# Performance work log

Measured on AMD Instinct MI355X. Metric: run time of the kernel, lower is better.

The kernel has to match this reference:

```python
import jax, jax.numpy as jnp
import numpy as np

HEADS = 8
UNITS = 1024
D_ATT = UNITS // HEADS  # 128
NEG_INF = -1e9  # matches Keras Attention additive causal mask


def setup_inputs() -> dict:
    key = jax.random.key(0)
    kx, kq, kk, kv, ko = jax.random.split(key, 5)
    B, T = 4, 2048
    scale = 0.02
    x = jax.random.normal(kx, (B, T, UNITS), dtype=jnp.float32)
    Wq = jax.random.normal(kq, (UNITS, HEADS * D_ATT), dtype=jnp.float32) * scale
    Wk = jax.random.normal(kk, (UNITS, HEADS * D_ATT), dtype=jnp.float32) * scale
    Wv = jax.random.normal(kv, (UNITS, D_ATT), dtype=jnp.float32) * scale
    Wo = jax.random.normal(ko, (D_ATT, UNITS), dtype=jnp.float32) * scale
    return {"x": x, "Wq": Wq, "Wk": Wk, "Wv": Wv, "Wo": Wo}


def reference(x, Wq, Wk, Wv, Wo):
    # TFT interpretable multi-head self-attention (inference; dropout inactive).
    B, T, U = x.shape
    H, d = HEADS, D_ATT
    scale = 1.0 / jnp.sqrt(jnp.asarray(d, x.dtype))  # query / sqrt(shape(key)[-1])
    q = (x @ Wq).reshape(B, T, H, d) * scale          # [B,T,H,d]
    k = (x @ Wk).reshape(B, T, H, d)                  # [B,T,H,d]
    v = x @ Wv                                        # [B,T,d], shared across heads
    scores = jnp.einsum("bthd,bshd->bhts", q, k)      # [B,H,T,T]
    causal = jnp.tril(jnp.ones((T, T), dtype=bool))   # [T,T]
    scores = jnp.where(causal, scores, jnp.asarray(NEG_INF, scores.dtype))
    w = jax.nn.softmax(scores, axis=-1)               # [B,H,T,T]
    out = jnp.einsum("bhts,bsd->bthd", w, v)          # [B,T,H,d]
    out = out.mean(axis=2) @ Wo                       # mean over heads -> Dense(units)
    attn = w.mean(axis=1)                             # mean attention over heads [B,T,T]
    return out, attn
```

## Files before the change

kernel.cpp:

```cpp
#include <hip/hip_runtime.h>

#define BATCH 4
#define TSEQ  2048
#define UNITS 1024
#define HEADS 8
#define DH    128
#define MROWS (BATCH*TSEQ)
#define NCAT  (2*UNITS + DH)

typedef short bf16x8 __attribute__((ext_vector_type(8)));
typedef short short4v __attribute__((ext_vector_type(4)));
typedef float f32x4  __attribute__((ext_vector_type(4)));

__device__ __forceinline__ short f2bf(float f){
    union { float f; unsigned u; } v; v.f = f;
    unsigned r = v.u + 0x7fff + ((v.u >> 16) & 1);
    return (short)(r >> 16);
}
__device__ __forceinline__ float redsum16(float v){
    #pragma unroll
    for (int m = 1; m < 16; m <<= 1) v += __shfl_xor(v, m);
    return v;
}
__device__ __forceinline__ void gload_lds16(const void* g, void* l){
    __builtin_amdgcn_global_load_lds(
        (const __attribute__((address_space(1))) void*)g,
        (__attribute__((address_space(3))) void*)l, 16, 0, 0);
}

#define QSCALE (0.08838834764831845f * 1.4426950408889634f)

__global__ __launch_bounds__(256) void xcast_kernel(const float* __restrict__ x,
                                                    short* __restrict__ Xbf)
{
    const int N = MROWS*UNITS/8;
    for (int i = blockIdx.x*256 + threadIdx.x; i < N; i += gridDim.x*256){
        f32x4 a = *(const f32x4*)(x + (size_t)i*8);
        f32x4 b = *(const f32x4*)(x + (size_t)i*8 + 4);
        bf16x8 o;
        o[0]=f2bf(a[0]); o[1]=f2bf(a[1]); o[2]=f2bf(a[2]); o[3]=f2bf(a[3]);
        o[4]=f2bf(b[0]); o[5]=f2bf(b[1]); o[6]=f2bf(b[2]); o[7]=f2bf(b[3]);
        *(bf16x8*)(Xbf + (size_t)i*8) = o;
    }
}

__global__ __launch_bounds__(256) void wtrans_kernel(
    const float* __restrict__ Wq, const float* __restrict__ Wk,
    const float* __restrict__ Wv, const float* __restrict__ Wo,
    short* __restrict__ WT, short* __restrict__ WoT)
{
    __shared__ float T_lds[64][65];
    const int tid = threadIdx.x;
    const int bid = blockIdx.x;
    if (bid < 544){
        const int nt = bid >> 4, kt = bid & 15;
        const int n0 = nt*64, k0 = kt*64;
        const float* src; int scol; float sc = 1.0f; int sstride = UNITS;
        if (n0 < UNITS){ src = Wq; scol = n0; sc = QSCALE; }
        else if (n0 < 2*UNITS){ src = Wk; scol = n0 - UNITS; }
        else { src = Wv; scol = n0 - 2*UNITS; sstride = DH; }
        const int ln = tid & 63, lk0 = tid >> 6;
        for (int kk = lk0; kk < 64; kk += 4)
            T_lds[kk][ln] = src[(size_t)(k0+kk)*sstride + scol + ln] * sc;
        __syncthreads();
        const int lk = tid & 63, ln0 = tid >> 6;
        for (int nn = ln0; nn < 64; nn += 4)
            WT[(size_t)(n0+nn)*UNITS + k0 + lk] = f2bf(T_lds[lk][nn]);
    } else {
        const int t = bid - 544;
        const int nt = t >> 1, dt = t & 1;
        const int n0 = nt*64, d0 = dt*64;
        const int ln = tid & 63, lk0 = tid >> 6;
        for (int dd = lk0; dd < 64; dd += 4)
            T_lds[dd][ln] = Wo[(size_t)(d0+dd)*UNITS + n0 + ln];
        __syncthreads();
        const int ld = tid & 63, ln0 = tid >> 6;
        for (int nn = ln0; nn < 64; nn += 4)
            WoT[(size_t)(n0+nn)*DH + d0 + ld] = f2bf(T_lds[ld][nn]);
    }
}

__global__ __launch_bounds__(256) void gemm_qkv_kernel(
    const short* __restrict__ X, const short* __restrict__ WT,
    short* __restrict__ Qbf, short* __restrict__ Kbf, short* __restrict__ Vt)
{
    __shared__ short A_lds[128][32];
    __shared__ short B_lds[128][32];
    const int tid = threadIdx.x;
    const int w = tid >> 6, l = tid & 63, lg = l >> 4, lr = l & 15;
    const int wm = w >> 1, wn = w & 1;
    const int n0 = blockIdx.x * 128;
    const int m0 = blockIdx.y * 128;
    const f32x4 fzero = {0.f, 0.f, 0.f, 0.f};
    f32x4 acc[4][4];
    #pragma unroll
    for (int i = 0; i < 4; i++)
        #pragma unroll
        for (int j = 0; j < 4; j++) acc[i][j] = fzero;

    const int srow = (l >> 2);
    const int scol = (l & 3) * 8;

    for (int k0 = 0; k0 < UNITS; k0 += 32){
        #pragma unroll
        for (int i = 0; i < 2; i++){
            int row = w*32 + i*16 + srow;
            gload_lds16(X  + (size_t)(m0+row)*UNITS + k0 + scol,
                        (char*)A_lds + ((w*2 + i) << 10));
            gload_lds16(WT + (size_t)(n0+row)*UNITS + k0 + scol,
                        (char*)B_lds + ((w*2 + i) << 10));
        }
        __syncthreads();
        bf16x8 af[4], bfr[4];
        #pragma unroll
        for (int mf = 0; mf < 4; mf++)
            af[mf] = *(const bf16x8*)(&A_lds[wm*64 + mf*16 + lr][lg*8]);
        #pragma unroll
        for (int nf = 0; nf < 4; nf++)
            bfr[nf] = *(const bf16x8*)(&B_lds[wn*64 + nf*16 + lr][lg*8]);
        #pragma unroll
        for (int mf = 0; mf < 4; mf++)
            #pragma unroll
            for (int nf = 0; nf < 4; nf++)
                acc[mf][nf] = __builtin_amdgcn_mfma_f32_16x16x32_bf16(
                    af[mf], bfr[nf], acc[mf][nf], 0, 0, 0);
        __syncthreads();
    }

    #pragma unroll
    for (int mf = 0; mf < 4; mf++){
        #pragma unroll
        for (int nf = 0; nf < 4; nf++){
            #pragma unroll
            for (int r = 0; r < 4; r++){
                int gr = m0 + wm*64 + mf*16 + lg*4 + r;
                int gc = n0 + wn*64 + nf*16 + lr;
                int b = gr >> 11, t = gr & 2047;
                short v = f2bf(acc[mf][nf][r]);
                if (gc < UNITS){
                    int h = gc >> 7, dd = gc & 127;
                    Qbf[(((size_t)(b*HEADS + h))*TSEQ + t)*DH + dd] = v;
                } else if (gc < 2*UNITS){
                    int h = (gc - UNITS) >> 7, dd = gc & 127;
                    Kbf[(((size_t)(b*HEADS + h))*TSEQ + t)*DH + dd] = v;
                } else {
                    int dd = gc - 2*UNITS;
                    Vt[((size_t)b*DH + dd)*TSEQ + t] = v;
                }
            }
        }
    }
}

__global__ __launch_bounds__(256) void stats_kernel(
    const short* __restrict__ Qbf, const short* __restrict__ Kbf,
    float* __restrict__ Lb)
{
    __shared__ short K_lds[2][64][136];
    const int tid = threadIdx.x;
    const int w = tid >> 6, l = tid & 63, lg = l >> 4, lr = l & 15;
    const int bh = blockIdx.y;
    const int qt = 31 - blockIdx.x;
    const int q0 = qt * 64;
    const short* Qh = Qbf + (size_t)bh*TSEQ*DH;
    const short* Kh = Kbf + (size_t)bh*TSEQ*DH;
    const f32x4 fzero = {0.f, 0.f, 0.f, 0.f};

    const int srow = tid >> 4;
    const int sc8  = tid & 15;

    const int qrow = q0 + w*16 + lr;
    bf16x8 aq[4];
    #pragma unroll
    for (int ks = 0; ks < 4; ks++)
        aq[ks] = *(const bf16x8*)(Qh + (size_t)qrow*DH + ks*32 + lg*8);

    bf16x8 kreg[4];
    #pragma unroll
    for (int i = 0; i < 4; i++)
        kreg[i] = *(const bf16x8*)(Kh + (size_t)(srow + i*16)*DH + sc8*8);
    #pragma unroll
    for (int i = 0; i < 4; i++)
        *(bf16x8*)(&K_lds[0][srow + i*16][sc8*8]) = kreg[i];
    __syncthreads();

    float lrow[4] = {0.f, 0.f, 0.f, 0.f};
    const int ntile = qt + 1;
    for (int t = 0; t < ntile; t++){
        const int cur = t & 1;
        if (t + 1 < ntile){
            const size_t base = (size_t)((t+1)*64 + srow)*DH + sc8*8;
            #pragma unroll
            for (int i = 0; i < 4; i++)
                kreg[i] = *(const bf16x8*)(Kh + base + (size_t)i*16*DH);
        }
        f32x4 sacc[4];
        #pragma unroll
        for (int nf = 0; nf < 4; nf++) sacc[nf] = fzero;
        __builtin_amdgcn_s_setprio(1);
        #pragma unroll
        for (int ks = 0; ks < 4; ks++){
            #pragma unroll
            for (int nf = 0; nf < 4; nf++){
                bf16x8 kb = *(const bf16x8*)(&K_lds[cur][nf*16 + lr][ks*32 + lg*8]);
                sacc[nf] = __builtin_amdgcn_mfma_f32_16x16x32_bf16(aq[ks], kb, sacc[nf], 0,0,0);
            }
        }
        __builtin_amdgcn_s_setprio(0);
        if (t == qt){
            #pragma unroll
            for (int nf = 0; nf < 4; nf++)
                #pragma unroll
                for (int r = 0; r < 4; r++)
                    if (nf*16 + lr > w*16 + lg*4 + r) sacc[nf][r] = -1e30f;
        }
        #pragma unroll
        for (int r = 0; r < 4; r++)
            lrow[r] += (exp2f(sacc[0][r]) + exp2f(sacc[1][r]))
                     + (exp2f(sacc[2][r]) + exp2f(sacc[3][r]));
        if (t + 1 < ntile){
            #pragma unroll
            for (int i = 0; i < 4; i++)
                *(bf16x8*)(&K_lds[cur ^ 1][srow + i*16][sc8*8]) = kreg[i];
        }
        __syncthreads();
    }
    #pragma unroll
    for (int r = 0; r < 4; r++) lrow[r] = redsum16(lrow[r]);
    if (lr == 0){
        #pragma unroll
        for (int r = 0; r < 4; r++){
            int t = q0 + w*16 + lg*4 + r;
            Lb[(size_t)bh*TSEQ + t] = 1.0f / lrow[r];
        }
    }
}

__global__ __launch_bounds__(256) void attn_kernel(
    const short* __restrict__ Qbf, const short* __restrict__ Kbf,
    const float* __restrict__ Lb, float* __restrict__ attn)
{
    const int tid = threadIdx.x;
    const int b = blockIdx.y;
    const int qt = blockIdx.x >> 5, kvt = blockIdx.x & 31;
    const int q0 = qt*128, k0 = kvt*64;
    float* At = attn + (size_t)b*TSEQ*TSEQ;

    if (k0 > q0 + 127){
        const f32x4 fz = {0.f, 0.f, 0.f, 0.f};
        #pragma unroll
        for (int i = 0; i < 8; i++){
            int c = tid + i*256;
            int row = c >> 4, c4 = c & 15;
            *(f32x4*)(At + (size_t)(q0+row)*TSEQ + k0 + c4*4) = fz;
        }
        return;
    }

    __shared__ short K_lds[2][64][136];
    const int w = tid >> 6, l = tid & 63, lg = l >> 4, lr = l & 15;
    const int srow = tid >> 4, sc8 = tid & 15;
    const f32x4 fzero = {0.f, 0.f, 0.f, 0.f};
    const size_t bh0 = (size_t)(b*HEADS)*TSEQ*DH;

    bf16x8 kreg[4];
    {
        const short* Kh = Kbf + bh0;
        #pragma unroll
        for (int i = 0; i < 4; i++)
            kreg[i] = *(const bf16x8*)(Kh + (size_t)(k0 + srow + i*16)*DH + sc8*8);
        #pragma unroll
        for (int i = 0; i < 4; i++)
            *(bf16x8*)(&K_lds[0][srow + i*16][sc8*8]) = kreg[i];
    }
    __syncthreads();

    f32x4 wacc[2][4];
    #pragma unroll
    for (int qf = 0; qf < 2; qf++)
        #pragma unroll
        for (int nf = 0; nf < 4; nf++) wacc[qf][nf] = fzero;

    for (int h = 0; h < HEADS; h++){
        const int cur = h & 1;
        if (h + 1 < HEADS){
            const short* Kn = Kbf + bh0 + (size_t)(h+1)*TSEQ*DH;
            #pragma unroll
            for (int i = 0; i < 4; i++)
                kreg[i] = *(const bf16x8*)(Kn + (size_t)(k0 + srow + i*16)*DH + sc8*8);
        }
        const short* Qh = Qbf + bh0 + (size_t)h*TSEQ*DH;
        bf16x8 aq[2][4];
        #pragma unroll
        for (int qf = 0; qf < 2; qf++)
            #pragma unroll
            for (int ks = 0; ks < 4; ks++)
                aq[qf][ks] = *(const bf16x8*)(Qh + (size_t)(q0 + w*32 + qf*16 + lr)*DH + ks*32 + lg*8);

        f32x4 sacc[2][4];
        #pragma unroll
        for (int qf = 0; qf < 2; qf++)
            #pragma unroll
            for (int nf = 0; nf < 4; nf++) sacc[qf][nf] = fzero;
        __builtin_amdgcn_s_setprio(1);
        #pragma unroll
        for (int ks = 0; ks < 4; ks++){
            #pragma unroll
            for (int nf = 0; nf < 4; nf++){
                bf16x8 kb = *(const bf16x8*)(&K_lds[cur][nf*16 + lr][ks*32 + lg*8]);
                sacc[0][nf] = __builtin_amdgcn_mfma_f32_16x16x32_bf16(aq[0][ks], kb, sacc[0][nf], 0,0,0);
                sacc[1][nf] = __builtin_amdgcn_mfma_f32_16x16x32_bf16(aq[1][ks], kb, sacc[1][nf], 0,0,0);
            }
        }
        __builtin_amdgcn_s_setprio(0);

        const float* Lh = Lb + ((size_t)(b*HEADS + h))*TSEQ;
        #pragma unroll
        for (int qf = 0; qf < 2; qf++){
            f32x4 rlh = *(const f32x4*)(Lh + q0 + w*32 + qf*16 + lg*4);
            #pragma unroll
            for (int nf = 0; nf < 4; nf++){
                #pragma unroll
                for (int r = 0; r < 4; r++){
                    int row = q0 + w*32 + qf*16 + lg*4 + r;
                    int col = k0 + nf*16 + lr;
                    float v = (col <= row) ? exp2f(sacc[qf][nf][r]) * rlh[r] : 0.f;
                    wacc[qf][nf][r] += v;
                }
            }
        }
        if (h + 1 < HEADS){
            #pragma unroll
            for (int i = 0; i < 4; i++)
                *(bf16x8*)(&K_lds[cur ^ 1][srow + i*16][sc8*8]) = kreg[i];
        }
        __syncthreads();
    }

    float* ob = (float*)&K_lds[0][0][0];
    #pragma unroll
    for (int qf = 0; qf < 2; qf++)
        #pragma unroll
        for (int nf = 0; nf < 4; nf++)
            #pragma unroll
            for (int r = 0; r < 4; r++)
                ob[(w*32 + qf*16 + lg*4 + r)*68 + nf*16 + lr] = wacc[qf][nf][r] * 0.125f;
    __syncthreads();
    #pragma unroll
    for (int i = 0; i < 8; i++){
        int c = tid + i*256;
        int row = c >> 4, c4 = c & 15;
        *(f32x4*)(At + (size_t)(q0+row)*TSEQ + k0 + c4*4) =
            *(const f32x4*)(ob + row*68 + c4*4);
    }
}

__global__ __launch_bounds__(256) void pv_kernel(
    const float* __restrict__ attn, const short* __restrict__ Vt,
    float* __restrict__ Obuf)
{
    __shared__ short A_lds[64][72];
    __shared__ short V_lds[128][72];
    const int tid = threadIdx.x;
    const int w = tid >> 6, l = tid & 63, lg = l >> 4, lr = l & 15;
    const int mt = blockIdx.x;
    const int ks0 = blockIdx.y;
    const int b = blockIdx.z;
    const int m0 = mt*64;
    const int kmax = m0 + 64;
    const int kbeg = ks0*512;
    if (kbeg >= kmax) return;
    const int kend = min(kbeg + 512, kmax);
    const int nact = (kmax + 511) >> 9;
    const float* Ab = attn + (size_t)b*TSEQ*TSEQ;
    const short* Vb = Vt + (size_t)b*DH*TSEQ;
    const f32x4 fzero = {0.f, 0.f, 0.f, 0.f};
    f32x4 acc[8];
    #pragma unroll
    for (int i = 0; i < 8; i++) acc[i] = fzero;

    for (int k0 = kbeg; k0 < kend; k0 += 64){
        #pragma unroll
        for (int i = 0; i < 4; i++){
            int c = tid + i*256;
            int row = c >> 4, c4 = c & 15;
            f32x4 av = *(const f32x4*)(Ab + (size_t)(m0+row)*TSEQ + k0 + c4*4);
            short4v o;
            o[0]=f2bf(av[0]); o[1]=f2bf(av[1]); o[2]=f2bf(av[2]); o[3]=f2bf(av[3]);
            *(short4v*)(&A_lds[row][c4*4]) = o;
        }
        #pragma unroll
        for (int i = 0; i < 4; i++){
            int c = tid + i*256;
            int row = c >> 3, c8 = c & 7;
            *(bf16x8*)(&V_lds[row][c8*8]) =
                *(const bf16x8*)(Vb + (size_t)row*TSEQ + k0 + c8*8);
        }
        __syncthreads();
        __builtin_amdgcn_s_setprio(1);
        #pragma unroll
        for (int ks = 0; ks < 2; ks++){
            bf16x8 a = *(const bf16x8*)(&A_lds[w*16 + lr][ks*32 + lg*8]);
            #pragma unroll
            for (int cg = 0; cg < 8; cg++){
                bf16x8 vb = *(const bf16x8*)(&V_lds[cg*16 + lr][ks*32 + lg*8]);
                acc[cg] = __builtin_amdgcn_mfma_f32_16x16x32_bf16(a, vb, acc[cg], 0,0,0);
            }
        }
        __builtin_amdgcn_s_setprio(0);
        __syncthreads();
    }
    #pragma unroll
    for (int cg = 0; cg < 8; cg++)
        #pragma unroll
        for (int r = 0; r < 4; r++){
            int row = m0 + w*16 + lg*4 + r, col = cg*16 + lr;
            float* p = &Obuf[((size_t)b*TSEQ + row)*DH + col];
            if (nact == 1) *p = acc[cg][r];
            else atomicAdd(p, acc[cg][r]);
        }
}

__global__ __launch_bounds__(256) void gemm_out_kernel(
    const float* __restrict__ Ob, const short* __restrict__ WoT,
    float* __restrict__ out)
{
    __shared__ short A_lds[128][40];
    __shared__ short B_lds[128][40];
    const int tid = threadIdx.x;
    const int w = tid >> 6, l = tid & 63, lg = l >> 4, lr = l & 15;
    const int wm = w >> 1, wn = w & 1;
    const int n0 = blockIdx.x * 128;
    const int m0 = blockIdx.y * 128;
    const f32x4 fzero = {0.f, 0.f, 0.f, 0.f};
    f32x4 acc[4][4];
    #pragma unroll
    for (int i = 0; i < 4; i++)
        #pragma unroll
        for (int j = 0; j < 4; j++) acc[i][j] = fzero;

    for (int k0 = 0; k0 < DH; k0 += 32){
        #pragma unroll
        for (int i = 0; i < 2; i++){
            int c = tid + i*256;
            int row = c >> 2, c8 = c & 3;
            f32x4 a0 = *(const f32x4*)(Ob + (size_t)(m0+row)*DH + k0 + c8*8);
            f32x4 a1 = *(const f32x4*)(Ob + (size_t)(m0+row)*DH + k0 + c8*8 + 4);
            bf16x8 o;
            o[0]=f2bf(a0[0]); o[1]=f2bf(a0[1]); o[2]=f2bf(a0[2]); o[3]=f2bf(a0[3]);
            o[4]=f2bf(a1[0]); o[5]=f2bf(a1[1]); o[6]=f2bf(a1[2]); o[7]=f2bf(a1[3]);
            *(bf16x8*)(&A_lds[row][c8*8]) = o;
            *(bf16x8*)(&B_lds[row][c8*8]) =
                *(const bf16x8*)(WoT + (size_t)(n0+row)*DH + k0 + c8*8);
        }
        __syncthreads();
        bf16x8 af[4], bfr[4];
        #pragma unroll
        for (int mf = 0; mf < 4; mf++)
            af[mf] = *(const bf16x8*)(&A_lds[wm*64 + mf*16 + lr][lg*8]);
        #pragma unroll
        for (int nf = 0; nf < 4; nf++)
            bfr[nf] = *(const bf16x8*)(&B_lds[wn*64 + nf*16 + lr][lg*8]);
        #pragma unroll
        for (int mf = 0; mf < 4; mf++)
            #pragma unroll
            for (int nf = 0; nf < 4; nf++)
                acc[mf][nf] = __builtin_amdgcn_mfma_f32_16x16x32_bf16(
                    af[mf], bfr[nf], acc[mf][nf], 0, 0, 0);
        __syncthreads();
    }
    #pragma unroll
    for (int mf = 0; mf < 4; mf++)
        #pragma unroll
        for (int nf = 0; nf < 4; nf++)
            #pragma unroll
            for (int r = 0; r < 4; r++){
                int gr = m0 + wm*64 + mf*16 + lg*4 + r;
                int gc = n0 + wn*64 + nf*16 + lr;
                out[(size_t)gr*UNITS + gc] = acc[mf][nf][r];
            }
}

extern "C" void kernel_launch(void* const* d_in, const int* in_sizes, int n_in,
                              void* d_out, int out_size, void* d_ws, size_t ws_size,
                              hipStream_t stream)
{
    const float* x  = (const float*)d_in[0];
    const float* Wq = (const float*)d_in[1];
    const float* Wk = (const float*)d_in[2];
    const float* Wv = (const float*)d_in[3];
    const float* Wo = (const float*)d_in[4];
    float* out  = (float*)d_out;
    float* attn = out + (size_t)MROWS*UNITS;

    char* ws = (char*)d_ws;
    short* Xbf = (short*)(ws);
    short* WT  = (short*)(ws + 16777216);
    short* Qbf = (short*)(ws + 21233664);
    short* Kbf = (short*)(ws + 38010880);
    short* Vt  = (short*)(ws + 54788096);
    float* Lb  = (float*)(ws + 57147392);
    short* WoT = (short*)(ws + 57409536);
    float* Obuf = (float*)ws;

    xcast_kernel<<<2048, 256, 0, stream>>>(x, Xbf);
    wtrans_kernel<<<576, 256, 0, stream>>>(Wq, Wk, Wv, Wo, WT, WoT);
    gemm_qkv_kernel<<<dim3(NCAT/128, MROWS/128), 256, 0, stream>>>(Xbf, WT, Qbf, Kbf, Vt);
    hipMemsetAsync(Obuf, 0, (size_t)MROWS*DH*sizeof(float), stream);
    stats_kernel<<<dim3(TSEQ/64, BATCH*HEADS), 256, 0, stream>>>(Qbf, Kbf, Lb);
    attn_kernel<<<dim3(16*32, BATCH), 256, 0, stream>>>(Qbf, Kbf, Lb, attn);
    pv_kernel<<<dim3(TSEQ/64, 4, BATCH), 256, 0, stream>>>(attn, Vt, Obuf);
    gemm_out_kernel<<<dim3(UNITS/128, MROWS/128), 256, 0, stream>>>(Obuf, WoT, out);
}
```

Baseline: 388.7 us.

## Swizzle K LDS layout and shrink attn tile to 64x64 with Q prefetch

Replaces the padded K shared-memory layout with an XOR-swizzled unpadded layout in both the stats and attn kernels, meant to avoid LDS bank conflicts while using less shared memory. The attn kernel's query tile shrinks from 128 to 64 rows with twice the grid, so fully masked tiles are skipped at finer granularity and more blocks fit per CU (launch bounds hint 5). It also prefetches the next head's Q fragment into registers and applies the causal mask only on diagonal tiles. The cost is that each K tile is reused across fewer query rows, so K global loads double.

New measurement: 376.1 us. 1.03x faster.

```diff
diff --git a/kernel.cpp b/kernel.cpp
--- a/kernel.cpp
+++ b/kernel.cpp
@@ -27,6 +27,8 @@
         (const __attribute__((address_space(1))) void*)g,
         (__attribute__((address_space(3))) void*)l, 16, 0, 0);
 }
+
+#define SWZB(r, cbyte) ((cbyte) ^ (((r) & 7) << 4))
 
 #define QSCALE (0.08838834764831845f * 1.4426950408889634f)
 
@@ -156,7 +158,7 @@
     const short* __restrict__ Qbf, const short* __restrict__ Kbf,
     float* __restrict__ Lb)
 {
-    __shared__ short K_lds[2][64][136];
+    __shared__ short K_lds[2][64][128];
     const int tid = threadIdx.x;
     const int w = tid >> 6, l = tid & 63, lg = l >> 4, lr = l & 15;
     const int bh = blockIdx.y;
@@ -180,8 +182,10 @@
     for (int i = 0; i < 4; i++)
         kreg[i] = *(const bf16x8*)(Kh + (size_t)(srow + i*16)*DH + sc8*8);
     #pragma unroll
-    for (int i = 0; i < 4; i++)
-        *(bf16x8*)(&K_lds[0][srow + i*16][sc8*8]) = kreg[i];
+    for (int i = 0; i < 4; i++){
+        int r = srow + i*16;
+        *(bf16x8*)((char*)&K_lds[0][0][0] + r*256 + SWZB(r, sc8*16)) = kreg[i];
+    }
     __syncthreads();
 
     float lrow[4] = {0.f, 0.f, 0.f, 0.f};
@@ -202,7 +206,9 @@
         for (int ks = 0; ks < 4; ks++){
             #pragma unroll
             for (int nf = 0; nf < 4; nf++){
-                bf16x8 kb = *(const bf16x8*)(&K_lds[cur][nf*16 + lr][ks*32 + lg*8]);
+                int r = nf*16 + lr;
+                bf16x8 kb = *(const bf16x8*)((char*)&K_lds[cur][0][0]
+                              + r*256 + SWZB(r, ks*64 + lg*16));
                 sacc[nf] = __builtin_amdgcn_mfma_f32_16x16x32_bf16(aq[ks], kb, sacc[nf], 0,0,0);
             }
         }
@@ -220,8 +226,10 @@
                      + (exp2f(sacc[2][r]) + exp2f(sacc[3][r]));
         if (t + 1 < ntile){
             #pragma unroll
-            for (int i = 0; i < 4; i++)
-                *(bf16x8*)(&K_lds[cur ^ 1][srow + i*16][sc8*8]) = kreg[i];
+            for (int i = 0; i < 4; i++){
+                int r = srow + i*16;
+                *(bf16x8*)((char*)&K_lds[cur ^ 1][0][0] + r*256 + SWZB(r, sc8*16)) = kreg[i];
+            }
         }
         __syncthreads();
     }
@@ -236,20 +244,20 @@
     }
 }
 
-__global__ __launch_bounds__(256) void attn_kernel(
+__global__ __launch_bounds__(256, 5) void attn_kernel(
     const short* __restrict__ Qbf, const short* __restrict__ Kbf,
     const float* __restrict__ Lb, float* __restrict__ attn)
 {
     const int tid = threadIdx.x;
     const int b = blockIdx.y;
     const int qt = blockIdx.x >> 5, kvt = blockIdx.x & 31;
-    const int q0 = qt*128, k0 = kvt*64;
+    const int q0 = qt*64, k0 = kvt*64;
     float* At = attn + (size_t)b*TSEQ*TSEQ;
 
-    if (k0 > q0 + 127){
+    if (kvt > qt){
         const f32x4 fz = {0.f, 0.f, 0.f, 0.f};
         #pragma unroll
-        for (int i = 0; i < 8; i++){
+        for (int i = 0; i < 4; i++){
             int c = tid + i*256;
             int row = c >> 4, c4 = c & 15;
             *(f32x4*)(At + (size_t)(q0+row)*TSEQ + k0 + c4*4) = fz;
@@ -257,7 +265,7 @@
         return;
     }
 
-    __shared__ short K_lds[2][64][136];
+    __shared__ short K_lds[2][64][128];
     const int w = tid >> 6, l = tid & 63, lg = l >> 4, lr = l & 15;
     const int srow = tid >> 4, sc8 = tid & 15;
     const f32x4 fzero = {0.f, 0.f, 0.f, 0.f};
@@ -270,84 +278,87 @@
         for (int i = 0; i < 4; i++)
             kreg[i] = *(const bf16x8*)(Kh + (size_t)(k0 + srow + i*16)*DH + sc8*8);
         #pragma unroll
-        for (int i = 0; i < 4; i++)
-            *(bf16x8*)(&K_lds[0][srow + i*16][sc8*8]) = kreg[i];
-    }
+        for (int i = 0; i < 4; i++){
+            int r = srow + i*16;
+            *(bf16x8*)((char*)&K_lds[0][0][0] + r*256 + SWZB(r, sc8*16)) = kreg[i];
+        }
+    }
+    bf16x8 aq[4];
+    #pragma unroll
+    for (int ks = 0; ks < 4; ks++)
+        aq[ks] = *(const bf16x8*)(Qbf + bh0 + (size_t)(q0 + w*16 + lr)*DH + ks*32 + lg*8);
     __syncthreads();
 
-    f32x4 wacc[2][4];
-    #pragma unroll
-    for (int qf = 0; qf < 2; qf++)
-        #pragma unroll
-        for (int nf = 0; nf < 4; nf++) wacc[qf][nf] = fzero;
+    f32x4 wacc[4];
+    #pragma unroll
+    for (int nf = 0; nf < 4; nf++) wacc[nf] = fzero;
 
     for (int h = 0; h < HEADS; h++){
         const int cur = h & 1;
+        bf16x8 aqn[4];
         if (h + 1 < HEADS){
-            const short* Kn = Kbf + bh0 + (size_t)(h+1)*TSEQ*DH;
+            const size_t bhn = bh0 + (size_t)(h+1)*TSEQ*DH;
+            const short* Kn = Kbf + bhn;
             #pragma unroll
             for (int i = 0; i < 4; i++)
                 kreg[i] = *(const bf16x8*)(Kn + (size_t)(k0 + srow + i*16)*DH + sc8*8);
-        }
-        const short* Qh = Qbf + bh0 + (size_t)h*TSEQ*DH;
-        bf16x8 aq[2][4];
-        #pragma unroll
-        for (int qf = 0; qf < 2; qf++)
+            const short* Qn = Qbf + bhn;
             #pragma unroll
             for (int ks = 0; ks < 4; ks++)
-                aq[qf][ks] = *(const bf16x8*)(Qh + (size_t)(q0 + w*32 + qf*16 + lr)*DH + ks*32 + lg*8);
-
-        f32x4 sacc[2][4];
-        #pragma unroll
-        for (int qf = 0; qf < 2; qf++)
-            #pragma unroll
-            for (int nf = 0; nf < 4; nf++) sacc[qf][nf] = fzero;
+                aqn[ks] = *(const bf16x8*)(Qn + (size_t)(q0 + w*16 + lr)*DH + ks*32 + lg*8);
+        }
+
+        f32x4 sacc[4];
+        #pragma unroll
+        for (int nf = 0; nf < 4; nf++) sacc[nf] = fzero;
         __builtin_amdgcn_s_setprio(1);
         #pragma unroll
         for (int ks = 0; ks < 4; ks++){
             #pragma unroll
             for (int nf = 0; nf < 4; nf++){
-                bf16x8 kb = *(const bf16x8*)(&K_lds[cur][nf*16 + lr][ks*32 + lg*8]);
-                sacc[0][nf] = __builtin_amdgcn_mfma_f32_16x16x32_bf16(aq[0][ks], kb, sacc[0][nf], 0,0,0);
-                sacc[1][nf] = __builtin_amdgcn_mfma_f32_16x16x32_bf16(aq[1][ks], kb, sacc[1][nf], 0,0,0);
+                int r = nf*16 + lr;
+                bf16x8 kb = *(const bf16x8*)((char*)&K_lds[cur][0][0]
+                              + r*256 + SWZB(r, ks*64 + lg*16));
+                sacc[nf] = __builtin_amdgcn_mfma_f32_16x16x32_bf16(aq[ks], kb, sacc[nf], 0,0,0);
             }
         }
         __builtin_amdgcn_s_setprio(0);
 
-        const float* Lh = Lb + ((size_t)(b*HEADS + h))*TSEQ;
-        #pragma unroll
-        for (int qf = 0; qf < 2; qf++){
-            f32x4 rlh = *(const f32x4*)(Lh + q0 + w*32 + qf*16 + lg*4);
-            #pragma unroll
-            for (int nf = 0; nf < 4; nf++){
+        if (kvt == qt){
+            #pragma unroll
+            for (int nf = 0; nf < 4; nf++)
                 #pragma unroll
-                for (int r = 0; r < 4; r++){
-                    int row = q0 + w*32 + qf*16 + lg*4 + r;
-                    int col = k0 + nf*16 + lr;
-                    float v = (col <= row) ? exp2f(sacc[qf][nf][r]) * rlh[r] : 0.f;
-                    wacc[qf][nf][r] += v;
-                }
-            }
-        }
+                for (int r = 0; r < 4; r++)
+                    if (nf*16 + lr > w*16 + lg*4 + r) sacc[nf][r] = -1e30f;
+        }
+        f32x4 rlh = *(const f32x4*)(Lb + ((size_t)(b*HEADS + h))*TSEQ + q0 + w*16 + lg*4);
+        #pragma unroll
+        for (int nf = 0; nf < 4; nf++)
+            #pragma unroll
+            for (int r = 0; r < 4; r++)
+                wacc[nf][r] += exp2f(sacc[nf][r]) * rlh[r];
+
         if (h + 1 < HEADS){
             #pragma unroll
-            for (int i = 0; i < 4; i++)
-                *(bf16x8*)(&K_lds[cur ^ 1][srow + i*16][sc8*8]) = kreg[i];
+            for (int i = 0; i < 4; i++){
+                int r = srow + i*16;
+                *(bf16x8*)((char*)&K_lds[cur ^ 1][0][0] + r*256 + SWZB(r, sc8*16)) = kreg[i];
+            }
+            #pragma unroll
+            for (int ks = 0; ks < 4; ks++) aq[ks] = aqn[ks];
         }
         __syncthreads();
     }
 
     float* ob = (float*)&K_lds[0][0][0];
     #pragma unroll
-    for (int qf = 0; qf < 2; qf++)
-        #pragma unroll
-        for (int nf = 0; nf < 4; nf++)
-            #pragma unroll
-            for (int r = 0; r < 4; r++)
-                ob[(w*32 + qf*16 + lg*4 + r)*68 + nf*16 + lr] = wacc[qf][nf][r] * 0.125f;
+    for (int nf = 0; nf < 4; nf++)
+        #pragma unroll
+        for (int r = 0; r < 4; r++)
+            ob[(w*16 + lg*4 + r)*68 + nf*16 + lr] = wacc[nf][r] * 0.125f;
     __syncthreads();
     #pragma unroll
-    for (int i = 0; i < 8; i++){
+    for (int i = 0; i < 4; i++){
         int c = tid + i*256;
         int row = c >> 4, c4 = c & 15;
         *(f32x4*)(At + (size_t)(q0+row)*TSEQ + k0 + c4*4) =
@@ -508,7 +519,7 @@
     gemm_qkv_kernel<<<dim3(NCAT/128, MROWS/128), 256, 0, stream>>>(Xbf, WT, Qbf, Kbf, Vt);
     hipMemsetAsync(Obuf, 0, (size_t)MROWS*DH*sizeof(float), stream);
     stats_kernel<<<dim3(TSEQ/64, BATCH*HEADS), 256, 0, stream>>>(Qbf, Kbf, Lb);
-    attn_kernel<<<dim3(16*32, BATCH), 256, 0, stream>>>(Qbf, Kbf, Lb, attn);
+    attn_kernel<<<dim3(32*32, BATCH), 256, 0, stream>>>(Qbf, Kbf, Lb, attn);
     pv_kernel<<<dim3(TSEQ/64, 4, BATCH), 256, 0, stream>>>(attn, Vt, Obuf);
     gemm_out_kernel<<<dim3(UNITS/128, MROWS/128), 256, 0, stream>>>(Obuf, WoT, out);
 }
```
